# Performance work log

Hardware: AMD Instinct MI355X
Metric: run time of the kernel (lower is better)

The kernel has to match this reference:

```python
import jax, jax.numpy as jnp
import numpy as np
import math

DIM = 1024
N_HEADS = 16
HEAD_DIM = DIM // N_HEADS
MAX_SEQ_LEN = 2048


def rope_tables(seq_len, head_dim):
    inv_freq = 1.0 / (10000.0 ** (jnp.arange(0, head_dim, 2, dtype=jnp.float32) / head_dim))
    t = jnp.arange(seq_len, dtype=jnp.float32)
    freqs = jnp.einsum('i,j->ij', t, inv_freq)          # [T, D/2]
    emb = jnp.concatenate([freqs, freqs], axis=-1)      # [T, D]
    return jnp.cos(emb), jnp.sin(emb)


def rotate_half(x):
    x1, x2 = jnp.split(x, 2, axis=-1)
    return jnp.concatenate([-x2, x1], axis=-1)


def setup_inputs() -> dict:
    key = jax.random.key(0)
    k1, k2, k3 = jax.random.split(key, 3)
    B, T = 4, 2048
    x = jax.random.normal(k1, (B, T, DIM), dtype=jnp.float32)
    # Linear(dim, 3*dim, bias=False) and Linear(dim, dim, bias=False); stored as [in, out]
    Wqkv = jax.random.normal(k2, (DIM, 3 * DIM), dtype=jnp.float32) * (1.0 / math.sqrt(DIM))
    Wproj = jax.random.normal(k3, (DIM, DIM), dtype=jnp.float32) * (1.0 / math.sqrt(DIM))
    return {"x": x, "Wqkv": Wqkv, "Wproj": Wproj}


def reference(x, Wqkv, Wproj):
    B, T, C = x.shape
    qkv = x @ Wqkv                                       # [B,T,3C]
    q, k, v = jnp.split(qkv, 3, axis=-1)
    # [B,T,C] -> [B,H,T,D]
    def to_heads(t_):
        return t_.reshape(B, T, N_HEADS, HEAD_DIM).transpose(0, 2, 1, 3)
    q, k, v = to_heads(q), to_heads(k), to_heads(v)
    cos, sin = rope_tables(T, HEAD_DIM)                  # [T,D]
    cos = cos[None, None, :, :]
    sin = sin[None, None, :, :]
    q = q * cos + rotate_half(q) * sin
    k = k * cos + rotate_half(k) * sin
    scale = 1.0 / math.sqrt(HEAD_DIM)
    att = jnp.einsum('bhqd,bhkd->bhqk', q, k) * scale    # [B,H,T,T]
    causal = jnp.triu(jnp.ones((T, T), dtype=bool), k=1)
    att = jnp.where(causal[None, None], -jnp.inf, att)
    att = jax.nn.softmax(att, axis=-1)
    y = jnp.einsum('bhqk,bhkd->bhqd', att, v)            # [B,H,T,D]
    y = y.transpose(0, 2, 1, 3).reshape(B, T, C)
    return y @ Wproj
```

## Files before the change

kernel.cpp:

```cpp
#include <hip/hip_runtime.h>
#include <hip/hip_bf16.h>

typedef unsigned short u16;
typedef __attribute__((ext_vector_type(8))) short short8;
typedef __attribute__((ext_vector_type(4))) float floatx4;

__device__ __forceinline__ u16 f2bf(float f) {
    union { float f; unsigned u; } v; v.f = f;
    unsigned r = v.u + 0x7fffu + ((v.u >> 16) & 1u);
    return (u16)(r >> 16);
}
__device__ __forceinline__ float bf2f(u16 b) {
    union { unsigned u; float f; } v; v.u = ((unsigned)b) << 16;
    return v.f;
}
__device__ __forceinline__ float fexp2(float x) {
#if __has_builtin(__builtin_amdgcn_exp2f)
    return __builtin_amdgcn_exp2f(x);
#else
    return exp2f(x);
#endif
}

__device__ __forceinline__ void async_load16(const void* g, void* l) {
    __builtin_amdgcn_global_load_lds(
        (const __attribute__((address_space(1))) unsigned int*)g,
        (__attribute__((address_space(3))) unsigned int*)l, 16, 0, 0);
}

#define B_   4
#define T_   2048
#define NH_  16
#define HD_  64
#define DIM_ 1024
#define M_   (B_ * T_)
#define NQKV (3 * DIM_)
#define LOG2E 1.4426950408889634f

__global__ void cvt_x(const float* __restrict__ in, u16* __restrict__ out) {
    int idx = blockIdx.x * 256 + threadIdx.x;
    float4 v = ((const float4*)in)[idx];
    ushort4 o;
    o.x = f2bf(v.x); o.y = f2bf(v.y); o.z = f2bf(v.z); o.w = f2bf(v.w);
    ((ushort4*)out)[idx] = o;
}

__global__ void transpose_cvt(const float* __restrict__ in, u16* __restrict__ out,
                              int R, int Cn) {
    __shared__ float tile[32][33];
    int c0 = blockIdx.x * 32, r0 = blockIdx.y * 32;
    int tx = threadIdx.x, ty = threadIdx.y;
#pragma unroll
    for (int i = 0; i < 4; ++i)
        tile[ty + i * 8][tx] = in[(size_t)(r0 + ty + i * 8) * Cn + c0 + tx];
    __syncthreads();
#pragma unroll
    for (int i = 0; i < 4; ++i)
        out[(size_t)(c0 + ty + i * 8) * R + r0 + tx] = f2bf(tile[tx][ty + i * 8]);
}

__global__ void rope_table(float* __restrict__ tabc, float* __restrict__ tabs) {
    int idx = blockIdx.x * 256 + threadIdx.x;
    if (idx >= T_ * 32) return;
    int t = idx >> 5, j = idx & 31;
    double invf = pow(10000.0, -(double)j / 32.0);
    double th = (double)t * invf;
    tabc[idx] = (float)cos(th);
    tabs[idx] = (float)sin(th);
}

__global__ void v_transpose(const u16* __restrict__ Vh, u16* __restrict__ Vt) {
    __shared__ u16 tile[64 * 68];
    const int tid = threadIdx.x;
    const int bh = blockIdx.y, b = bh >> 4, h = bh & 15;
    const int t0 = blockIdx.x * 64;
    {
        int lr = tid >> 2;
        int lc = tid & 3;
        const u16* src = Vh + ((size_t)(b * T_ + t0 + lr)) * DIM_ + h * HD_;
#pragma unroll
        for (int j = 0; j < 4; ++j) {
            int c = (lc + j * 4) * 4;
            *(uint2*)&tile[lr * 68 + c] = *(const uint2*)(src + c);
        }
    }
    __syncthreads();
    {
        int d2 = tid >> 3, tseg = tid & 7;
        u16 lo8[8], hi8[8];
#pragma unroll
        for (int j = 0; j < 8; ++j) {
            unsigned w = *(const unsigned*)&tile[(tseg * 8 + j) * 68 + d2 * 2];
            lo8[j] = (u16)(w & 0xffffu);
            hi8[j] = (u16)(w >> 16);
        }
        size_t ob = ((size_t)bh * HD_ + 2 * d2) * T_ + t0 + tseg * 8;
        *(uint4*)(Vt + ob) = *(const uint4*)lo8;
        *(uint4*)(Vt + ob + T_) = *(const uint4*)hi8;
    }
}


__global__ __launch_bounds__(256) void gemm_qkv(const u16* __restrict__ A,
                                                const u16* __restrict__ Bt,
                                                const float* __restrict__ tabc,
                                                const float* __restrict__ tabs,
                                                u16* __restrict__ Qo,
                                                u16* __restrict__ Ko,
                                                u16* __restrict__ Vh) {
    __shared__ __align__(16) u16 Asl[128 * 64];
    __shared__ __align__(16) u16 Bsl[128 * 64];
    const int tid = threadIdx.x;
    const int wave = tid >> 6, lane = tid & 63;
    const int ln15 = lane & 15, quad = lane >> 4;
    const int m0 = blockIdx.y * 128, n0 = blockIdx.x * 128;
    const int wm = (wave & 1) * 64, wn = (wave >> 1) * 64;
    const int l8 = lane & 7, ld8 = lane >> 3;
    const int sgc = (l8 ^ ld8) * 8;
    const int K = DIM_;

    floatx4 acc[4][4] = {};

    for (int k0 = 0; k0 < K; k0 += 64) {
#pragma unroll
        for (int it = 0; it < 4; ++it) {
            int rb = wave * 32 + it * 8;
            async_load16(A  + (size_t)(m0 + rb + ld8) * K + k0 + sgc, &Asl[rb * 64]);
            async_load16(Bt + (size_t)(n0 + rb + ld8) * K + k0 + sgc, &Bsl[rb * 64]);
        }
        __syncthreads();
#pragma unroll
        for (int kk = 0; kk < 64; kk += 32) {
            const int c4 = kk >> 3;
            short8 af[4], bfm[4];
#pragma unroll
            for (int i = 0; i < 4; ++i) {
                int row = wm + i * 16 + ln15;
                af[i] = *(const short8*)&Asl[row * 64 + (((c4 + quad) ^ (row & 7)) << 3)];
            }
#pragma unroll
            for (int jj = 0; jj < 4; ++jj) {
                int row = wn + jj * 16 + ln15;
                bfm[jj] = *(const short8*)&Bsl[row * 64 + (((c4 + quad) ^ (row & 7)) << 3)];
            }
#pragma unroll
            for (int i = 0; i < 4; ++i)
#pragma unroll
                for (int jj = 0; jj < 4; ++jj)
                    acc[i][jj] = __builtin_amdgcn_mfma_f32_16x16x32_bf16(
                        af[i], bfm[jj], acc[i][jj], 0, 0, 0);
        }
        __syncthreads();
    }

    const int sel = n0 >> 10;
    if (sel == 2) {
#pragma unroll
        for (int i = 0; i < 4; ++i)
#pragma unroll
            for (int jj = 0; jj < 4; ++jj)
#pragma unroll
                for (int r = 0; r < 4; ++r) {
                    int m = m0 + wm + i * 16 + quad * 4 + r;
                    int n = (n0 & 1023) + wn + jj * 16 + ln15;
                    Vh[(size_t)m * DIM_ + n] = f2bf(acc[i][jj][r]);
                }
    } else {
        u16* outp = sel ? Ko : Qo;
        const float scale = sel ? 1.0f : 0.125f * LOG2E;
        const int h = ((n0 & 1023) + wn) >> 6;
#pragma unroll
        for (int i = 0; i < 4; ++i)
#pragma unroll
            for (int jjl = 0; jjl < 2; ++jjl) {
                floatx4 xl = acc[i][jjl], xh = acc[i][jjl + 2];
                int j = jjl * 16 + ln15;
#pragma unroll
                for (int r = 0; r < 4; ++r) {
                    int m = m0 + wm + i * 16 + quad * 4 + r;
                    int t = m & (T_ - 1), b = m >> 11;
                    float cs = tabc[t * 32 + j], sn = tabs[t * 32 + j];
                    float ol = (xl[r] * cs - xh[r] * sn) * scale;
                    float oh = (xh[r] * cs + xl[r] * sn) * scale;
                    size_t ob = ((size_t)((b * NH_ + h) * T_ + t)) * HD_ + j;
                    outp[ob] = f2bf(ol);
                    outp[ob + 32] = f2bf(oh);
                }
            }
    }
}

__global__ __launch_bounds__(256) void gemm_bt_f32(const u16* __restrict__ A,
                                                   const u16* __restrict__ Bt,
                                                   float* __restrict__ C,
                                                   int M, int N, int K) {
    __shared__ __align__(16) u16 Asl[128 * 64];
    __shared__ __align__(16) u16 Bsl[128 * 64];
    const int tid = threadIdx.x;
    const int wave = tid >> 6, lane = tid & 63;
    const int ln15 = lane & 15, quad = lane >> 4;
    const int m0 = blockIdx.y * 128, n0 = blockIdx.x * 128;
    const int wm = (wave & 1) * 64, wn = (wave >> 1) * 64;
    const int l8 = lane & 7, ld8 = lane >> 3;
    const int sgc = (l8 ^ ld8) * 8;

    floatx4 acc[4][4] = {};

    for (int k0 = 0; k0 < K; k0 += 64) {
#pragma unroll
        for (int it = 0; it < 4; ++it) {
            int rb = wave * 32 + it * 8;
            async_load16(A  + (size_t)(m0 + rb + ld8) * K + k0 + sgc, &Asl[rb * 64]);
            async_load16(Bt + (size_t)(n0 + rb + ld8) * K + k0 + sgc, &Bsl[rb * 64]);
        }
        __syncthreads();
#pragma unroll
        for (int kk = 0; kk < 64; kk += 32) {
            const int c4 = kk >> 3;
            short8 af[4], bfm[4];
#pragma unroll
            for (int i = 0; i < 4; ++i) {
                int row = wm + i * 16 + ln15;
                af[i] = *(const short8*)&Asl[row * 64 + (((c4 + quad) ^ (row & 7)) << 3)];
            }
#pragma unroll
            for (int jj = 0; jj < 4; ++jj) {
                int row = wn + jj * 16 + ln15;
                bfm[jj] = *(const short8*)&Bsl[row * 64 + (((c4 + quad) ^ (row & 7)) << 3)];
            }
#pragma unroll
            for (int i = 0; i < 4; ++i)
#pragma unroll
                for (int jj = 0; jj < 4; ++jj)
                    acc[i][jj] = __builtin_amdgcn_mfma_f32_16x16x32_bf16(
                        af[i], bfm[jj], acc[i][jj], 0, 0, 0);
        }
        __syncthreads();
    }
#pragma unroll
    for (int i = 0; i < 4; ++i)
#pragma unroll
        for (int jj = 0; jj < 4; ++jj)
#pragma unroll
            for (int r = 0; r < 4; ++r) {
                int m = m0 + wm + i * 16 + quad * 4 + r;
                int n = n0 + wn + jj * 16 + ln15;
                C[(size_t)m * N + n] = acc[i][jj][r];
            }
}

__global__ __launch_bounds__(256, 4) void attn_kernel(const u16* __restrict__ Q,
                                                      const u16* __restrict__ Kh,
                                                      const u16* __restrict__ Vt,
                                                      u16* __restrict__ Y) {
    __shared__ __align__(16) u16 Kl[2][64 * 64];
    __shared__ __align__(16) u16 Vl[2][64 * 64];
    __shared__ __align__(16) u16 Pl[4][16 * 64];
    const int tid = threadIdx.x, wave = tid >> 6, lane = tid & 63;
    const int ln15 = lane & 15, quad = lane >> 4;
    const int p = blockIdx.x;
    const int bh = blockIdx.y;
    const int b = bh >> 4, h = bh & 15;
    const int l8 = lane & 7, ld8 = lane >> 3;
    const int sgc = l8 ^ ld8;

    const u16* kbase = Kh + (size_t)bh * T_ * HD_;
    const u16* vbase = Vt + (size_t)bh * HD_ * T_;
    const short8 ones = {0x3F80, 0x3F80, 0x3F80, 0x3F80,
                         0x3F80, 0x3F80, 0x3F80, 0x3F80};
    const int srow = wave * 16;

#pragma unroll
    for (int half = 0; half < 2; ++half) {
        const int tidx = half ? p : (31 - p);
        const int q0 = tidx * 64;
        const int bm = q0 + wave * 16;

        const u16* qp = Q + ((size_t)bh * T_ + bm + ln15) * HD_;
        short8 qf0 = *(const short8*)(qp + quad * 8);
        short8 qf1 = *(const short8*)(qp + 32 + quad * 8);

        floatx4 o[5] = {};

        __syncthreads();
#pragma unroll
        for (int it = 0; it < 2; ++it) {
            int r = srow + it * 8;
            async_load16(kbase + (size_t)(r + ld8) * HD_ + sgc * 8, &Kl[0][r * 64]);
            async_load16(vbase + (size_t)(r + ld8) * T_ + sgc * 8, &Vl[0][r * 64]);
        }

        for (int kt = 0; kt <= tidx; ++kt) {
            const int cur = kt & 1;
            __syncthreads();
            if (kt < tidx) {
                const int kn = (kt + 1) * 64;
#pragma unroll
                for (int it = 0; it < 2; ++it) {
                    int r = srow + it * 8;
                    async_load16(kbase + (size_t)(kn + r + ld8) * HD_ + sgc * 8,
                                 &Kl[cur ^ 1][r * 64]);
                    async_load16(vbase + (size_t)(r + ld8) * T_ + kn + sgc * 8,
                                 &Vl[cur ^ 1][r * 64]);
                }
            }
            floatx4 s[4] = {};
#pragma unroll
            for (int nt = 0; nt < 4; ++nt) {
                int row = nt * 16 + ln15;
                short8 kf0 = *(const short8*)&Kl[cur][row * 64 + ((quad ^ (row & 7)) << 3)];
                short8 kf1 = *(const short8*)&Kl[cur][row * 64 + (((4 + quad) ^ (row & 7)) << 3)];
                s[nt] = __builtin_amdgcn_mfma_f32_16x16x32_bf16(qf0, kf0, s[nt], 0, 0, 0);
                s[nt] = __builtin_amdgcn_mfma_f32_16x16x32_bf16(qf1, kf1, s[nt], 0, 0, 0);
            }
            if (kt == tidx) {
#pragma unroll
                for (int nt = 0; nt < 4; ++nt) {
                    int key = nt * 16 + ln15, lim = wave * 16 + quad * 4;
#pragma unroll
                    for (int r = 0; r < 4; ++r)
                        s[nt][r] = (key > lim + r) ? 0.f : fexp2(s[nt][r]);
                }
            } else {
#pragma unroll
                for (int nt = 0; nt < 4; ++nt)
#pragma unroll
                    for (int r = 0; r < 4; ++r) s[nt][r] = fexp2(s[nt][r]);
            }
            u16* pw = Pl[wave];
#pragma unroll
            for (int nt = 0; nt < 4; ++nt) {
                int kc = nt * 2 + (ln15 >> 3), k7 = ln15 & 7;
#pragma unroll
                for (int r = 0; r < 4; ++r) {
                    int row = quad * 4 + r;
                    pw[row * 64 + ((kc ^ (row & 7)) << 3) + k7] = f2bf(s[nt][r]);
                }
            }
            short8 pf0 = *(const short8*)&pw[ln15 * 64 + ((quad ^ (ln15 & 7)) << 3)];
            short8 pf1 = *(const short8*)&pw[ln15 * 64 + (((4 + quad) ^ (ln15 & 7)) << 3)];
#pragma unroll
            for (int nt = 0; nt < 4; ++nt) {
                int row = nt * 16 + ln15;
                short8 vf0 = *(const short8*)&Vl[cur][row * 64 + ((quad ^ (row & 7)) << 3)];
                short8 vf1 = *(const short8*)&Vl[cur][row * 64 + (((4 + quad) ^ (row & 7)) << 3)];
                o[nt] = __builtin_amdgcn_mfma_f32_16x16x32_bf16(pf0, vf0, o[nt], 0, 0, 0);
                o[nt] = __builtin_amdgcn_mfma_f32_16x16x32_bf16(pf1, vf1, o[nt], 0, 0, 0);
            }
            o[4] = __builtin_amdgcn_mfma_f32_16x16x32_bf16(pf0, ones, o[4], 0, 0, 0);
            o[4] = __builtin_amdgcn_mfma_f32_16x16x32_bf16(pf1, ones, o[4], 0, 0, 0);
        }
#pragma unroll
        for (int r = 0; r < 4; ++r) {
            float inv = 1.f / o[4][r];
            int row = bm + quad * 4 + r;
            u16* yp = Y + ((size_t)(b * T_ + row)) * DIM_ + h * HD_;
#pragma unroll
            for (int nt = 0; nt < 4; ++nt)
                yp[nt * 16 + ln15] = f2bf(o[nt][r] * inv);
        }
    }
}

extern "C" void kernel_launch(void* const* d_in, const int* in_sizes, int n_in,
                              void* d_out, int out_size, void* d_ws, size_t ws_size,
                              hipStream_t stream) {
    const float* x     = (const float*)d_in[0];
    const float* Wqkv  = (const float*)d_in[1];
    const float* Wproj = (const float*)d_in[2];
    float* out = (float*)d_out;
    char* ws = (char*)d_ws;

    const size_t SZ_XB  = (size_t)M_ * DIM_ * 2;
    const size_t SZ_WQT = (size_t)NQKV * DIM_ * 2;
    const size_t SZ_WPT = (size_t)DIM_ * DIM_ * 2;
    const size_t SZ_Q   = SZ_XB;
    const size_t SZ_TAB = (size_t)T_ * 32 * 4;

    u16*   xb   = (u16*)(ws);
    u16*   wqt  = (u16*)(ws + SZ_XB);
    u16*   wpt  = (u16*)(ws + SZ_XB + SZ_WQT);
    u16*   qb   = (u16*)(ws + SZ_XB + SZ_WQT + SZ_WPT);
    u16*   kb   = (u16*)(ws + SZ_XB + SZ_WQT + SZ_WPT + SZ_Q);
    u16*   vhb  = (u16*)(ws + SZ_XB + SZ_WQT + SZ_WPT + 2 * SZ_Q);
    u16*   vtb  = (u16*)(ws + SZ_XB + SZ_WQT + SZ_WPT + 3 * SZ_Q);
    float* tabc = (float*)(ws + SZ_XB + SZ_WQT + SZ_WPT + 4 * SZ_Q);
    float* tabs = (float*)(ws + SZ_XB + SZ_WQT + SZ_WPT + 4 * SZ_Q + SZ_TAB);
    u16*   yb   = xb;

    rope_table<<<(T_ * 32 + 255) / 256, 256, 0, stream>>>(tabc, tabs);
    cvt_x<<<(M_ * DIM_ / 4) / 256, 256, 0, stream>>>(x, xb);
    transpose_cvt<<<dim3(NQKV / 32, DIM_ / 32), dim3(32, 8), 0, stream>>>(Wqkv, wqt, DIM_, NQKV);
    transpose_cvt<<<dim3(DIM_ / 32, DIM_ / 32), dim3(32, 8), 0, stream>>>(Wproj, wpt, DIM_, DIM_);
    gemm_qkv<<<dim3(NQKV / 128, M_ / 128), 256, 0, stream>>>(xb, wqt, tabc, tabs, qb, kb, vhb);
    v_transpose<<<dim3(T_ / 64, B_ * NH_), 256, 0, stream>>>(vhb, vtb);
    attn_kernel<<<dim3(16, B_ * NH_), 256, 0, stream>>>(qb, kb, vtb, yb);
    gemm_bt_f32<<<dim3(DIM_ / 128, M_ / 128), 256, 0, stream>>>(yb, wpt, out, M_, DIM_, DIM_);
}
```

Measured before the change: 268.2 us.

## Stage QKV epilogue through LDS and share K/V tiles across paired query tiles

The QKV GEMM epilogue now writes the RoPE-rotated, bf16-converted results into swizzled shared memory first, then emits coalesced 16-byte stores to the Q/K/V head layouts instead of scattered 2-byte stores. The attention kernel now processes both paired query tiles (31-p and p) in one pass over the key/value tiles, so each K/V tile is loaded into LDS once and used for both query tiles, where before each half streamed its keys separately. The block-to-tile mapping is also rotated by head index to spread the causal work. This raises register use from two sets of accumulators and Q fragments, which could lower occupancy under the 4-blocks launch bound.

```diff
diff --git a/kernel.cpp b/kernel.cpp
--- a/kernel.cpp
+++ b/kernel.cpp
@@ -9,10 +9,6 @@
     union { float f; unsigned u; } v; v.f = f;
     unsigned r = v.u + 0x7fffu + ((v.u >> 16) & 1u);
     return (u16)(r >> 16);
-}
-__device__ __forceinline__ float bf2f(u16 b) {
-    union { unsigned u; float f; } v; v.u = ((unsigned)b) << 16;
-    return v.f;
 }
 __device__ __forceinline__ float fexp2(float x) {
 #if __has_builtin(__builtin_amdgcn_exp2f)
@@ -100,7 +96,6 @@
     }
 }
 
-
 __global__ __launch_bounds__(256) void gemm_qkv(const u16* __restrict__ A,
                                                 const u16* __restrict__ Bt,
                                                 const float* __restrict__ tabc,
@@ -108,8 +103,9 @@
                                                 u16* __restrict__ Qo,
                                                 u16* __restrict__ Ko,
                                                 u16* __restrict__ Vh) {
-    __shared__ __align__(16) u16 Asl[128 * 64];
-    __shared__ __align__(16) u16 Bsl[128 * 64];
+    __shared__ __align__(16) u16 smem[2 * 128 * 64];
+    u16* Asl = smem;
+    u16* Bsl = smem + 128 * 64;
     const int tid = threadIdx.x;
     const int wave = tid >> 6, lane = tid & 63;
     const int ln15 = lane & 15, quad = lane >> 4;
@@ -153,40 +149,57 @@
         __syncthreads();
     }
 
+    u16* Es = smem;
     const int sel = n0 >> 10;
+    auto es_put = [&](int row, int col, u16 v) {
+        int c = col >> 3;
+        int pc = (c & 8) | ((c & 7) ^ (row & 7));
+        Es[row * 128 + pc * 8 + (col & 7)] = v;
+    };
     if (sel == 2) {
 #pragma unroll
         for (int i = 0; i < 4; ++i)
 #pragma unroll
             for (int jj = 0; jj < 4; ++jj)
 #pragma unroll
+                for (int r = 0; r < 4; ++r)
+                    es_put(wm + i * 16 + quad * 4 + r, wn + jj * 16 + ln15,
+                           f2bf(acc[i][jj][r]));
+    } else {
+        const float scale = sel ? 1.0f : 0.125f * LOG2E;
+#pragma unroll
+        for (int i = 0; i < 4; ++i)
+#pragma unroll
+            for (int jjl = 0; jjl < 2; ++jjl) {
+                int j = jjl * 16 + ln15;
+#pragma unroll
                 for (int r = 0; r < 4; ++r) {
-                    int m = m0 + wm + i * 16 + quad * 4 + r;
-                    int n = (n0 & 1023) + wn + jj * 16 + ln15;
-                    Vh[(size_t)m * DIM_ + n] = f2bf(acc[i][jj][r]);
+                    int row = wm + i * 16 + quad * 4 + r;
+                    int t = (m0 + row) & (T_ - 1);
+                    float cs = tabc[t * 32 + j], sn = tabs[t * 32 + j];
+                    float xl = acc[i][jjl][r], xh = acc[i][jjl + 2][r];
+                    es_put(row, wn + j,      f2bf((xl * cs - xh * sn) * scale));
+                    es_put(row, wn + j + 32, f2bf((xh * cs + xl * sn) * scale));
                 }
-    } else {
-        u16* outp = sel ? Ko : Qo;
-        const float scale = sel ? 1.0f : 0.125f * LOG2E;
-        const int h = ((n0 & 1023) + wn) >> 6;
-#pragma unroll
-        for (int i = 0; i < 4; ++i)
-#pragma unroll
-            for (int jjl = 0; jjl < 2; ++jjl) {
-                floatx4 xl = acc[i][jjl], xh = acc[i][jjl + 2];
-                int j = jjl * 16 + ln15;
-#pragma unroll
-                for (int r = 0; r < 4; ++r) {
-                    int m = m0 + wm + i * 16 + quad * 4 + r;
-                    int t = m & (T_ - 1), b = m >> 11;
-                    float cs = tabc[t * 32 + j], sn = tabs[t * 32 + j];
-                    float ol = (xl[r] * cs - xh[r] * sn) * scale;
-                    float oh = (xh[r] * cs + xl[r] * sn) * scale;
-                    size_t ob = ((size_t)((b * NH_ + h) * T_ + t)) * HD_ + j;
-                    outp[ob] = f2bf(ol);
-                    outp[ob + 32] = f2bf(oh);
-                }
-            }
+            }
+    }
+    __syncthreads();
+    const int bb = m0 >> 11;
+    u16* outqk = (sel == 1) ? Ko : Qo;
+#pragma unroll
+    for (int k = 0; k < 8; ++k) {
+        int cid = tid + k * 256;
+        int row = cid >> 4, c = cid & 15;
+        int pc = (c & 8) | ((c & 7) ^ (row & 7));
+        uint4 v = *(const uint4*)&Es[row * 128 + pc * 8];
+        if (sel == 2) {
+            *(uint4*)&Vh[(size_t)(m0 + row) * DIM_ + (n0 & 1023) + c * 8] = v;
+        } else {
+            int h = ((n0 & 1023) >> 6) + (c >> 3);
+            int d = (c & 7) * 8;
+            int t = (m0 + row) & (T_ - 1);
+            *(uint4*)&outqk[((size_t)(bb * NH_ + h) * T_ + t) * HD_ + d] = v;
+        }
     }
 }
 
@@ -258,11 +271,12 @@
     __shared__ __align__(16) u16 Pl[4][16 * 64];
     const int tid = threadIdx.x, wave = tid >> 6, lane = tid & 63;
     const int ln15 = lane & 15, quad = lane >> 4;
-    const int p = blockIdx.x;
+    const int p = (blockIdx.x + (blockIdx.y >> 2)) & 15;
     const int bh = blockIdx.y;
     const int b = bh >> 4, h = bh & 15;
     const int l8 = lane & 7, ld8 = lane >> 3;
     const int sgc = l8 ^ ld8;
+    const int tA = 31 - p, tB = p;
 
     const u16* kbase = Kh + (size_t)bh * T_ * HD_;
     const u16* vbase = Vt + (size_t)bh * HD_ * T_;
@@ -270,90 +284,97 @@
                          0x3F80, 0x3F80, 0x3F80, 0x3F80};
     const int srow = wave * 16;
 
-#pragma unroll
-    for (int half = 0; half < 2; ++half) {
-        const int tidx = half ? p : (31 - p);
-        const int q0 = tidx * 64;
-        const int bm = q0 + wave * 16;
-
-        const u16* qp = Q + ((size_t)bh * T_ + bm + ln15) * HD_;
-        short8 qf0 = *(const short8*)(qp + quad * 8);
-        short8 qf1 = *(const short8*)(qp + 32 + quad * 8);
-
-        floatx4 o[5] = {};
-
+    const u16* qpA = Q + ((size_t)bh * T_ + tA * 64 + srow + ln15) * HD_;
+    const u16* qpB = Q + ((size_t)bh * T_ + tB * 64 + srow + ln15) * HD_;
+    short8 qfA0 = *(const short8*)(qpA + quad * 8);
+    short8 qfA1 = *(const short8*)(qpA + 32 + quad * 8);
+    short8 qfB0 = *(const short8*)(qpB + quad * 8);
+    short8 qfB1 = *(const short8*)(qpB + 32 + quad * 8);
+
+    floatx4 oA[5] = {}, oB[5] = {};
+    int cur = 0;
+
+#pragma unroll
+    for (int it = 0; it < 2; ++it) {
+        int r = srow + it * 8;
+        async_load16(kbase + (size_t)(r + ld8) * HD_ + sgc * 8, &Kl[0][r * 64]);
+        async_load16(vbase + (size_t)(r + ld8) * T_ + sgc * 8, &Vl[0][r * 64]);
+    }
+
+    auto process = [&](short8 qf0, short8 qf1, floatx4* o, bool diag) {
+        floatx4 s[4] = {};
+#pragma unroll
+        for (int nt = 0; nt < 4; ++nt) {
+            int row = nt * 16 + ln15;
+            short8 kf0 = *(const short8*)&Kl[cur][row * 64 + ((quad ^ (row & 7)) << 3)];
+            short8 kf1 = *(const short8*)&Kl[cur][row * 64 + (((4 + quad) ^ (row & 7)) << 3)];
+            s[nt] = __builtin_amdgcn_mfma_f32_16x16x32_bf16(qf0, kf0, s[nt], 0, 0, 0);
+            s[nt] = __builtin_amdgcn_mfma_f32_16x16x32_bf16(qf1, kf1, s[nt], 0, 0, 0);
+        }
+        if (diag) {
+#pragma unroll
+            for (int nt = 0; nt < 4; ++nt) {
+                int key = nt * 16 + ln15, lim = srow + quad * 4;
+#pragma unroll
+                for (int r = 0; r < 4; ++r)
+                    s[nt][r] = (key > lim + r) ? 0.f : fexp2(s[nt][r]);
+            }
+        } else {
+#pragma unroll
+            for (int nt = 0; nt < 4; ++nt)
+#pragma unroll
+                for (int r = 0; r < 4; ++r) s[nt][r] = fexp2(s[nt][r]);
+        }
+        u16* pw = Pl[wave];
+#pragma unroll
+        for (int nt = 0; nt < 4; ++nt) {
+            int kc = nt * 2 + (ln15 >> 3), k7 = ln15 & 7;
+#pragma unroll
+            for (int r = 0; r < 4; ++r) {
+                int row = quad * 4 + r;
+                pw[row * 64 + ((kc ^ (row & 7)) << 3) + k7] = f2bf(s[nt][r]);
+            }
+        }
+        short8 pf0 = *(const short8*)&pw[ln15 * 64 + ((quad ^ (ln15 & 7)) << 3)];
+        short8 pf1 = *(const short8*)&pw[ln15 * 64 + (((4 + quad) ^ (ln15 & 7)) << 3)];
+#pragma unroll
+        for (int nt = 0; nt < 4; ++nt) {
+            int row = nt * 16 + ln15;
+            short8 vf0 = *(const short8*)&Vl[cur][row * 64 + ((quad ^ (row & 7)) << 3)];
+            short8 vf1 = *(const short8*)&Vl[cur][row * 64 + (((4 + quad) ^ (row & 7)) << 3)];
+            o[nt] = __builtin_amdgcn_mfma_f32_16x16x32_bf16(pf0, vf0, o[nt], 0, 0, 0);
+            o[nt] = __builtin_amdgcn_mfma_f32_16x16x32_bf16(pf1, vf1, o[nt], 0, 0, 0);
+        }
+        o[4] = __builtin_amdgcn_mfma_f32_16x16x32_bf16(pf0, ones, o[4], 0, 0, 0);
+        o[4] = __builtin_amdgcn_mfma_f32_16x16x32_bf16(pf1, ones, o[4], 0, 0, 0);
+    };
+
+    for (int kt = 0; kt <= tA; ++kt) {
+        cur = kt & 1;
         __syncthreads();
-#pragma unroll
-        for (int it = 0; it < 2; ++it) {
-            int r = srow + it * 8;
-            async_load16(kbase + (size_t)(r + ld8) * HD_ + sgc * 8, &Kl[0][r * 64]);
-            async_load16(vbase + (size_t)(r + ld8) * T_ + sgc * 8, &Vl[0][r * 64]);
-        }
-
-        for (int kt = 0; kt <= tidx; ++kt) {
-            const int cur = kt & 1;
-            __syncthreads();
-            if (kt < tidx) {
-                const int kn = (kt + 1) * 64;
-#pragma unroll
-                for (int it = 0; it < 2; ++it) {
-                    int r = srow + it * 8;
-                    async_load16(kbase + (size_t)(kn + r + ld8) * HD_ + sgc * 8,
-                                 &Kl[cur ^ 1][r * 64]);
-                    async_load16(vbase + (size_t)(r + ld8) * T_ + kn + sgc * 8,
-                                 &Vl[cur ^ 1][r * 64]);
-                }
-            }
-            floatx4 s[4] = {};
-#pragma unroll
-            for (int nt = 0; nt < 4; ++nt) {
-                int row = nt * 16 + ln15;
-                short8 kf0 = *(const short8*)&Kl[cur][row * 64 + ((quad ^ (row & 7)) << 3)];
-                short8 kf1 = *(const short8*)&Kl[cur][row * 64 + (((4 + quad) ^ (row & 7)) << 3)];
-                s[nt] = __builtin_amdgcn_mfma_f32_16x16x32_bf16(qf0, kf0, s[nt], 0, 0, 0);
-                s[nt] = __builtin_amdgcn_mfma_f32_16x16x32_bf16(qf1, kf1, s[nt], 0, 0, 0);
-            }
-            if (kt == tidx) {
-#pragma unroll
-                for (int nt = 0; nt < 4; ++nt) {
-                    int key = nt * 16 + ln15, lim = wave * 16 + quad * 4;
-#pragma unroll
-                    for (int r = 0; r < 4; ++r)
-                        s[nt][r] = (key > lim + r) ? 0.f : fexp2(s[nt][r]);
-                }
-            } else {
-#pragma unroll
-                for (int nt = 0; nt < 4; ++nt)
-#pragma unroll
-                    for (int r = 0; r < 4; ++r) s[nt][r] = fexp2(s[nt][r]);
-            }
-            u16* pw = Pl[wave];
-#pragma unroll
-            for (int nt = 0; nt < 4; ++nt) {
-                int kc = nt * 2 + (ln15 >> 3), k7 = ln15 & 7;
-#pragma unroll
-                for (int r = 0; r < 4; ++r) {
-                    int row = quad * 4 + r;
-                    pw[row * 64 + ((kc ^ (row & 7)) << 3) + k7] = f2bf(s[nt][r]);
-                }
-            }
-            short8 pf0 = *(const short8*)&pw[ln15 * 64 + ((quad ^ (ln15 & 7)) << 3)];
-            short8 pf1 = *(const short8*)&pw[ln15 * 64 + (((4 + quad) ^ (ln15 & 7)) << 3)];
-#pragma unroll
-            for (int nt = 0; nt < 4; ++nt) {
-                int row = nt * 16 + ln15;
-                short8 vf0 = *(const short8*)&Vl[cur][row * 64 + ((quad ^ (row & 7)) << 3)];
-                short8 vf1 = *(const short8*)&Vl[cur][row * 64 + (((4 + quad) ^ (row & 7)) << 3)];
-                o[nt] = __builtin_amdgcn_mfma_f32_16x16x32_bf16(pf0, vf0, o[nt], 0, 0, 0);
-                o[nt] = __builtin_amdgcn_mfma_f32_16x16x32_bf16(pf1, vf1, o[nt], 0, 0, 0);
-            }
-            o[4] = __builtin_amdgcn_mfma_f32_16x16x32_bf16(pf0, ones, o[4], 0, 0, 0);
-            o[4] = __builtin_amdgcn_mfma_f32_16x16x32_bf16(pf1, ones, o[4], 0, 0, 0);
-        }
+        if (kt < tA) {
+            const int kn = (kt + 1) * 64;
+#pragma unroll
+            for (int it = 0; it < 2; ++it) {
+                int r = srow + it * 8;
+                async_load16(kbase + (size_t)(kn + r + ld8) * HD_ + sgc * 8,
+                             &Kl[cur ^ 1][r * 64]);
+                async_load16(vbase + (size_t)(r + ld8) * T_ + kn + sgc * 8,
+                             &Vl[cur ^ 1][r * 64]);
+            }
+        }
+        process(qfA0, qfA1, oA, kt == tA);
+        if (kt <= tB) process(qfB0, qfB1, oB, kt == tB);
+    }
+
+#pragma unroll
+    for (int sel = 0; sel < 2; ++sel) {
+        const floatx4* o = sel ? oB : oA;
+        const int base = (sel ? tB : tA) * 64 + srow;
 #pragma unroll
         for (int r = 0; r < 4; ++r) {
             float inv = 1.f / o[4][r];
-            int row = bm + quad * 4 + r;
+            int row = base + quad * 4 + r;
             u16* yp = Y + ((size_t)(b * T_ + row)) * DIM_ + h * HD_;
 #pragma unroll
             for (int nt = 0; nt < 4; ++nt)
```

Result: slower. 409.9 us (+52.8%).
